# Optimization experiments

Measured on AMD Instinct MI355X. Metric: run time of the kernel, lower is better.

The kernel has to match this reference:

```python
import jax, jax.numpy as jnp
import numpy as np

N = 32768   # total nodes
E = 524288  # directed edges
F = 128     # input features
H = 128     # hidden width
G = 64      # graphs in batch (N//G = 512 nodes each)


def _lin(key, fan_in, fan_out):
    return jax.random.normal(key, (fan_in, fan_out), jnp.float32) / np.sqrt(fan_in)


def setup_inputs() -> dict:
    key = jax.random.key(0)
    ks = jax.random.split(key, 16)
    d = {}
    d["x"] = jax.random.normal(ks[0], (N, F), jnp.float32)
    d["edge_index"] = jax.random.randint(ks[1], (2, E), 0, N, dtype=jnp.int64)
    d["batch"] = (jnp.arange(N, dtype=jnp.int64) // (N // G))  # sorted, equal-size graphs
    # GCNConv 1 / 2
    d["W1"] = _lin(ks[2], F, H); d["b1"] = jnp.zeros((H,), jnp.float32)
    d["W2"] = _lin(ks[3], H, H); d["b2"] = jnp.zeros((H,), jnp.float32)
    # GraphSelfAttention (per-graph Q/K/V self-attention)
    d["Wq"] = _lin(ks[4], H, H); d["bq"] = jnp.zeros((H,), jnp.float32)
    d["Wk"] = _lin(ks[5], H, H); d["bk"] = jnp.zeros((H,), jnp.float32)
    d["Wv"] = _lin(ks[6], H, H); d["bv"] = jnp.zeros((H,), jnp.float32)
    # MLP head
    d["Wh1"] = _lin(ks[7], H, 64); d["bh1"] = jnp.zeros((64,), jnp.float32)
    d["Wh2"] = _lin(ks[8], 64, 1); d["bh2"] = jnp.zeros((1,), jnp.float32)
    return d


def gcn_conv(x, src, dst, W, b, num_nodes):
    """PyG-style GCNConv: D^{-1/2}(A+I)D^{-1/2} x W + b (self-loops already in src/dst)."""
    h = x @ W                                                    # [N, out]
    deg = jax.ops.segment_sum(jnp.ones_like(dst, dtype=h.dtype), dst,
                              num_segments=num_nodes)            # [N]
    dinv = jax.lax.rsqrt(jnp.maximum(deg, 1.0))
    norm = dinv[src] * dinv[dst]                                 # [E+N]
    msg = h[src] * norm[:, None]                                 # gather
    return jax.ops.segment_sum(msg, dst, num_segments=num_nodes) + b  # scatter-add


def reference(x, edge_index, batch, W1, b1, W2, b2, Wq, bq, Wk, bk, Wv, bv,
              Wh1, bh1, Wh2, bh2):
    num_nodes = x.shape[0]
    loop = jnp.arange(num_nodes, dtype=edge_index.dtype)
    src = jnp.concatenate([edge_index[0], loop])
    dst = jnp.concatenate([edge_index[1], loop])

    x = x.astype(jnp.float32)
    h = jax.nn.relu(gcn_conv(x, src, dst, W1, b1, num_nodes))    # dropout: eval mode (identity)
    h = jax.nn.relu(gcn_conv(h, src, dst, W2, b2, num_nodes))

    # batch = arange // n (equal-size sorted segments) -> dense reshape is exact
    n = num_nodes // G
    hg = h.reshape(G, n, H)                                      # [G, n, H]
    q = hg @ Wq + bq
    k = hg @ Wk + bk
    v = hg @ Wv + bv
    scores = jnp.einsum("gnd,gmd->gnm", q, k) / np.sqrt(H)       # [G, n, n]
    attn = jax.nn.softmax(scores, axis=-1)
    pooled = jnp.einsum("gnm,gmd->gnd", attn, v).mean(axis=1)    # [G, H]

    out = jax.nn.relu(pooled @ Wh1 + bh1) @ Wh2 + bh2            # [G, 1]
    return out
```

## Files before the change

kernel.cpp:

```cpp
#include <hip/hip_runtime.h>
#include <hip/hip_fp16.h>
#include <hip/hip_bf16.h>

#define NN 32768
#define GG 64
#define NPG 512
#define HD 128
#define MAXD 64
#define RSQRT_H 0.08838834764831845f

typedef _Float16 f16;
typedef __attribute__((ext_vector_type(8))) _Float16 f16x8;
typedef __attribute__((ext_vector_type(4))) float f32x4;

__global__ void k_fill(const int* __restrict__ src, const int* __restrict__ dst,
                       int* __restrict__ cursor, int* __restrict__ ell, int E) {
    int e = blockIdx.x * 256 + threadIdx.x;
    if (e < E) {
        int d = dst[e];
        int slot = atomicAdd(&cursor[d], 1);
        if (slot < MAXD) ell[d * MAXD + slot] = src[e];
    }
}

#define FMA_ROW(r, av, wv) \
    acc[r][0] += (av)*(wv).x; acc[r][1] += (av)*(wv).y; \
    acc[r][2] += (av)*(wv).z; acc[r][3] += (av)*(wv).w;

__global__ __launch_bounds__(256) void k_gemm_h(
    const float* __restrict__ A, const float* __restrict__ W,
    __half* __restrict__ out, int M)
{
    __shared__ float Al[64][132];
    __shared__ float Wt[128][68];
    int t = threadIdx.x;
    int row0 = blockIdx.x * 64;
    int col0 = blockIdx.y * 64;

    const float4* A4 = (const float4*)(A + (size_t)row0 * HD);
#pragma unroll
    for (int i = 0; i < 8; ++i) {
        int idx = t + 256 * i;
        *(float4*)&Al[idx >> 5][(idx & 31) * 4] = A4[idx];
    }
    const float4* W4 = (const float4*)W;
#pragma unroll
    for (int i = 0; i < 8; ++i) {
        int idx = t + 256 * i;
        int k = idx >> 4, cq = idx & 15;
        *(float4*)&Wt[k][cq * 4] = W4[k * 32 + (col0 >> 2) + cq];
    }
    __syncthreads();

    int cg = t & 15, rg = t >> 4;
    float acc[4][4] = {{0.f}};
#pragma unroll 2
    for (int kk = 0; kk < 128; kk += 4) {
        float4 a0 = *(const float4*)&Al[rg * 4 + 0][kk];
        float4 a1 = *(const float4*)&Al[rg * 4 + 1][kk];
        float4 a2 = *(const float4*)&Al[rg * 4 + 2][kk];
        float4 a3 = *(const float4*)&Al[rg * 4 + 3][kk];
        float4 w0 = *(const float4*)&Wt[kk + 0][cg * 4];
        float4 w1 = *(const float4*)&Wt[kk + 1][cg * 4];
        float4 w2 = *(const float4*)&Wt[kk + 2][cg * 4];
        float4 w3 = *(const float4*)&Wt[kk + 3][cg * 4];
        FMA_ROW(0, a0.x, w0) FMA_ROW(0, a0.y, w1) FMA_ROW(0, a0.z, w2) FMA_ROW(0, a0.w, w3)
        FMA_ROW(1, a1.x, w0) FMA_ROW(1, a1.y, w1) FMA_ROW(1, a1.z, w2) FMA_ROW(1, a1.w, w3)
        FMA_ROW(2, a2.x, w0) FMA_ROW(2, a2.y, w1) FMA_ROW(2, a2.z, w2) FMA_ROW(2, a2.w, w3)
        FMA_ROW(3, a3.x, w0) FMA_ROW(3, a3.y, w1) FMA_ROW(3, a3.z, w2) FMA_ROW(3, a3.w, w3)
    }
#pragma unroll
    for (int r = 0; r < 4; ++r) {
        int row = row0 + rg * 4 + r;
        __half2 p01, p23;
        p01.x = __float2half(acc[r][0]); p01.y = __float2half(acc[r][1]);
        p23.x = __float2half(acc[r][2]); p23.y = __float2half(acc[r][3]);
        __half2* o = (__half2*)&out[(size_t)row * HD + col0 + cg * 4];
        o[0] = p01; o[1] = p23;
    }
}

__global__ __launch_bounds__(256) void k_gemm_qk(
    const float* __restrict__ A,
    const float* __restrict__ Wq, const float* __restrict__ bq,
    const float* __restrict__ Wk, const float* __restrict__ bk,
    __half* __restrict__ qout, __half* __restrict__ kout)
{
    __shared__ float Al[64][132];
    __shared__ float Wt[128][68];
    int t = threadIdx.x;
    int row0 = blockIdx.x * 64;
    int col0 = blockIdx.y * 64;
    int cg = t & 15, rg = t >> 4;

    const float4* A4 = (const float4*)(A + (size_t)row0 * HD);
#pragma unroll
    for (int i = 0; i < 8; ++i) {
        int idx = t + 256 * i;
        *(float4*)&Al[idx >> 5][(idx & 31) * 4] = A4[idx];
    }
    const float4* Wq4 = (const float4*)Wq;
#pragma unroll
    for (int i = 0; i < 8; ++i) {
        int idx = t + 256 * i;
        int k = idx >> 4, cq = idx & 15;
        *(float4*)&Wt[k][cq * 4] = Wq4[k * 32 + (col0 >> 2) + cq];
    }
    __syncthreads();

    {
        float acc[4][4] = {{0.f}};
#pragma unroll 2
        for (int kk = 0; kk < 128; kk += 4) {
            float4 a0 = *(const float4*)&Al[rg * 4 + 0][kk];
            float4 a1 = *(const float4*)&Al[rg * 4 + 1][kk];
            float4 a2 = *(const float4*)&Al[rg * 4 + 2][kk];
            float4 a3 = *(const float4*)&Al[rg * 4 + 3][kk];
            float4 w0 = *(const float4*)&Wt[kk + 0][cg * 4];
            float4 w1 = *(const float4*)&Wt[kk + 1][cg * 4];
            float4 w2 = *(const float4*)&Wt[kk + 2][cg * 4];
            float4 w3 = *(const float4*)&Wt[kk + 3][cg * 4];
            FMA_ROW(0, a0.x, w0) FMA_ROW(0, a0.y, w1) FMA_ROW(0, a0.z, w2) FMA_ROW(0, a0.w, w3)
            FMA_ROW(1, a1.x, w0) FMA_ROW(1, a1.y, w1) FMA_ROW(1, a1.z, w2) FMA_ROW(1, a1.w, w3)
            FMA_ROW(2, a2.x, w0) FMA_ROW(2, a2.y, w1) FMA_ROW(2, a2.z, w2) FMA_ROW(2, a2.w, w3)
            FMA_ROW(3, a3.x, w0) FMA_ROW(3, a3.y, w1) FMA_ROW(3, a3.z, w2) FMA_ROW(3, a3.w, w3)
        }
        int c = col0 + cg * 4;
        float b0 = bq[c], b1 = bq[c+1], b2 = bq[c+2], b3 = bq[c+3];
#pragma unroll
        for (int r = 0; r < 4; ++r) {
            int row = row0 + rg * 4 + r;
            __half2 p01, p23;
            p01.x = __float2half(acc[r][0] + b0); p01.y = __float2half(acc[r][1] + b1);
            p23.x = __float2half(acc[r][2] + b2); p23.y = __float2half(acc[r][3] + b3);
            __half2* o = (__half2*)&qout[(size_t)row * HD + c];
            o[0] = p01; o[1] = p23;
        }
    }
    __syncthreads();
    const float4* Wk4 = (const float4*)Wk;
#pragma unroll
    for (int i = 0; i < 8; ++i) {
        int idx = t + 256 * i;
        int k = idx >> 4, cq = idx & 15;
        *(float4*)&Wt[k][cq * 4] = Wk4[k * 32 + (col0 >> 2) + cq];
    }
    __syncthreads();

    float acc[4][4] = {{0.f}};
#pragma unroll 2
    for (int kk = 0; kk < 128; kk += 4) {
        float4 a0 = *(const float4*)&Al[rg * 4 + 0][kk];
        float4 a1 = *(const float4*)&Al[rg * 4 + 1][kk];
        float4 a2 = *(const float4*)&Al[rg * 4 + 2][kk];
        float4 a3 = *(const float4*)&Al[rg * 4 + 3][kk];
        float4 w0 = *(const float4*)&Wt[kk + 0][cg * 4];
        float4 w1 = *(const float4*)&Wt[kk + 1][cg * 4];
        float4 w2 = *(const float4*)&Wt[kk + 2][cg * 4];
        float4 w3 = *(const float4*)&Wt[kk + 3][cg * 4];
        FMA_ROW(0, a0.x, w0) FMA_ROW(0, a0.y, w1) FMA_ROW(0, a0.z, w2) FMA_ROW(0, a0.w, w3)
        FMA_ROW(1, a1.x, w0) FMA_ROW(1, a1.y, w1) FMA_ROW(1, a1.z, w2) FMA_ROW(1, a1.w, w3)
        FMA_ROW(2, a2.x, w0) FMA_ROW(2, a2.y, w1) FMA_ROW(2, a2.z, w2) FMA_ROW(2, a2.w, w3)
        FMA_ROW(3, a3.x, w0) FMA_ROW(3, a3.y, w1) FMA_ROW(3, a3.z, w2) FMA_ROW(3, a3.w, w3)
    }
    {
        int c = col0 + cg * 4;
        float b0 = bk[c], b1 = bk[c+1], b2 = bk[c+2], b3 = bk[c+3];
#pragma unroll
        for (int r = 0; r < 4; ++r) {
            int row = row0 + rg * 4 + r;
            __half2 p01, p23;
            p01.x = __float2half(acc[r][0] + b0); p01.y = __float2half(acc[r][1] + b1);
            p23.x = __float2half(acc[r][2] + b2); p23.y = __float2half(acc[r][3] + b3);
            __half2* o = (__half2*)&kout[(size_t)row * HD + c];
            o[0] = p01; o[1] = p23;
        }
    }
}

__global__ __launch_bounds__(256) void k_agg(
    const __half* __restrict__ tmat, const int* __restrict__ cursor,
    const int* __restrict__ ell, const float* __restrict__ bias,
    float* __restrict__ hout)
{
    int t = threadIdx.x;
    int i = blockIdx.x * 4 + (t >> 6);
    int lane = t & 63;
    int cnt = min(cursor[i], MAXD);
    float di = rsqrtf((float)(cnt + 1));
    float2 sv = __half22float2(((const __half2*)(tmat + (size_t)i * HD))[lane]);
    float acc0 = sv.x * (di * di);
    float acc1 = sv.y * (di * di);
    const int* row = ell + (size_t)i * MAXD;
    int e = 0;
    for (; e + 2 <= cnt; e += 2) {
        int s0 = row[e], s1 = row[e + 1];
        float w0 = rsqrtf((float)(min(cursor[s0], MAXD) + 1)) * di;
        float w1 = rsqrtf((float)(min(cursor[s1], MAXD) + 1)) * di;
        float2 v0 = __half22float2(((const __half2*)(tmat + (size_t)s0 * HD))[lane]);
        float2 v1 = __half22float2(((const __half2*)(tmat + (size_t)s1 * HD))[lane]);
        acc0 += v0.x * w0 + v1.x * w1;
        acc1 += v0.y * w0 + v1.y * w1;
    }
    if (e < cnt) {
        int s0 = row[e];
        float w0 = rsqrtf((float)(min(cursor[s0], MAXD) + 1)) * di;
        float2 v0 = __half22float2(((const __half2*)(tmat + (size_t)s0 * HD))[lane]);
        acc0 += v0.x * w0;
        acc1 += v0.y * w0;
    }
    int f = lane * 2;
    *(float2*)&hout[(size_t)i * HD + f] =
        make_float2(fmaxf(acc0 + bias[f], 0.f), fmaxf(acc1 + bias[f + 1], 0.f));
}

__global__ __launch_bounds__(256, 2) void k_attn(
    const __half* __restrict__ qh,
    const __half* __restrict__ kh,
    float* __restrict__ wpart)
{
    __shared__ f16 Kl[64][136];
    __shared__ float wlp[4][512];
    int t = threadIdx.x;
    int g = blockIdx.x >> 3;
    int qt = blockIdx.x & 7;
    int w = t >> 6, lane = t & 63;
    int lr = lane & 15, lu = lane >> 4;
    int qrow0 = g * NPG + qt * 64;

    f16x8 aq[4];
    {
        const f16* qp = (const f16*)qh + (size_t)(qrow0 + w * 16 + lr) * HD + lu * 8;
#pragma unroll
        for (int ks = 0; ks < 4; ++ks)
            aq[ks] = *(const f16x8*)(qp + ks * 32);
    }

    f32x4 p[8][4];
#pragma unroll
    for (int mt = 0; mt < 8; ++mt) {
        __syncthreads();
        {
            const float4* ks4 = (const float4*)(kh + (size_t)(g * NPG + mt * 64) * HD);
#pragma unroll
            for (int i = 0; i < 4; ++i) {
                int idx = t + 256 * i;
                int row = idx >> 4, cq = idx & 15;
                *(float4*)&Kl[row][cq * 8] = ks4[row * 16 + cq];
            }
        }
        __syncthreads();
#pragma unroll
        for (int ni = 0; ni < 4; ++ni) {
            f32x4 acc = {0.f, 0.f, 0.f, 0.f};
#pragma unroll
            for (int ks = 0; ks < 4; ++ks) {
                f16x8 b = *(const f16x8*)&Kl[ni * 16 + lr][ks * 32 + lu * 8];
                acc = __builtin_amdgcn_mfma_f32_16x16x32_f16(aq[ks], b, acc, 0, 0, 0);
            }
            p[mt][ni] = acc;
        }
    }

    float mrow[4], linv[4];
#pragma unroll
    for (int j = 0; j < 4; ++j) {
        float m = p[0][0][j];
#pragma unroll
        for (int mt = 0; mt < 8; ++mt)
#pragma unroll
            for (int ni = 0; ni < 4; ++ni) m = fmaxf(m, p[mt][ni][j]);
        m = fmaxf(m, __shfl_xor(m, 1));
        m = fmaxf(m, __shfl_xor(m, 2));
        m = fmaxf(m, __shfl_xor(m, 4));
        m = fmaxf(m, __shfl_xor(m, 8));
        mrow[j] = m;
    }
#pragma unroll
    for (int mt = 0; mt < 8; ++mt)
#pragma unroll
        for (int ni = 0; ni < 4; ++ni)
#pragma unroll
            for (int j = 0; j < 4; ++j)
                p[mt][ni][j] = __expf((p[mt][ni][j] - mrow[j]) * RSQRT_H);
#pragma unroll
    for (int j = 0; j < 4; ++j) {
        float l = 0.f;
#pragma unroll
        for (int mt = 0; mt < 8; ++mt)
#pragma unroll
            for (int ni = 0; ni < 4; ++ni) l += p[mt][ni][j];
        l += __shfl_xor(l, 1);
        l += __shfl_xor(l, 2);
        l += __shfl_xor(l, 4);
        l += __shfl_xor(l, 8);
        linv[j] = 1.f / l;
    }
#pragma unroll
    for (int mt = 0; mt < 8; ++mt)
#pragma unroll
        for (int ni = 0; ni < 4; ++ni) {
            float pc = p[mt][ni][0] * linv[0] + p[mt][ni][1] * linv[1]
                     + p[mt][ni][2] * linv[2] + p[mt][ni][3] * linv[3];
            pc += __shfl_xor(pc, 16);
            pc += __shfl_xor(pc, 32);
            if (lu == 0) wlp[w][mt * 64 + ni * 16 + lr] = pc;
        }
    __syncthreads();
    float* wp = wpart + ((size_t)(g * 8 + qt)) * NPG;
    wp[t] = (wlp[0][t] + wlp[1][t] + wlp[2][t] + wlp[3][t]) * (1.f / NPG);
    wp[t + 256] = (wlp[0][t + 256] + wlp[1][t + 256] + wlp[2][t + 256]
                 + wlp[3][t + 256]) * (1.f / NPG);
}

__global__ __launch_bounds__(128) void k_pool(
    const float* __restrict__ wpart, const float* __restrict__ h,
    float* __restrict__ upart)
{
    __shared__ float wloc[64];
    int b = blockIdx.x;
    int g = b >> 3, ch = b & 7;
    int t = threadIdx.x;
    if (t < 64) {
        float w = 0.f;
#pragma unroll
        for (int qt = 0; qt < 8; ++qt)
            w += wpart[((size_t)(g * 8 + qt)) * NPG + ch * 64 + t];
        wloc[t] = w;
    }
    __syncthreads();
    const float* hg = h + ((size_t)g * NPG + ch * 64) * HD;
    float u = 0.f;
#pragma unroll 4
    for (int m = 0; m < 64; ++m) u += wloc[m] * hg[m * HD + t];
    upart[(size_t)(ch * GG + g) * HD + t] = u;
}

__global__ __launch_bounds__(128) void k_head2(
    const float* __restrict__ upart,
    const float* __restrict__ Wv, const float* __restrict__ bv,
    const float* __restrict__ Wh1, const float* __restrict__ bh1,
    const float* __restrict__ Wh2, const float* __restrict__ bh2,
    float* __restrict__ out)
{
    __shared__ float ul[128];
    __shared__ float pl[128];
    __shared__ float r1l[64];
    int g = blockIdx.x, t = threadIdx.x;
    float ud = 0.f;
#pragma unroll
    for (int ch = 0; ch < 8; ++ch) ud += upart[(size_t)(ch * GG + g) * HD + t];
    ul[t] = ud;
    __syncthreads();
    float pv = bv[t];
    for (int d = 0; d < HD; ++d) pv += ul[d] * Wv[d * HD + t];
    pl[t] = pv;
    __syncthreads();
    if (t < 64) {
        float r1 = bh1[t];
        for (int d = 0; d < HD; ++d) r1 += pl[d] * Wh1[d * 64 + t];
        r1l[t] = fmaxf(r1, 0.f);
    }
    __syncthreads();
    if (t == 0) {
        float o = bh2[0];
        for (int j = 0; j < 64; ++j) o += r1l[j] * Wh2[j];
        out[g] = o;
    }
}

extern "C" void kernel_launch(void* const* d_in, const int* in_sizes, int n_in,
                              void* d_out, int out_size, void* d_ws, size_t ws_size,
                              hipStream_t stream) {
    const float* x   = (const float*)d_in[0];
    const int* edge  = (const int*)d_in[1];
    const float* W1  = (const float*)d_in[3];
    const float* b1  = (const float*)d_in[4];
    const float* W2  = (const float*)d_in[5];
    const float* b2  = (const float*)d_in[6];
    const float* Wq  = (const float*)d_in[7];
    const float* bq  = (const float*)d_in[8];
    const float* Wk  = (const float*)d_in[9];
    const float* bk  = (const float*)d_in[10];
    const float* Wv  = (const float*)d_in[11];
    const float* bv  = (const float*)d_in[12];
    const float* Wh1 = (const float*)d_in[13];
    const float* bh1 = (const float*)d_in[14];
    const float* Wh2 = (const float*)d_in[15];
    const float* bh2 = (const float*)d_in[16];
    float* out = (float*)d_out;

    int E = in_sizes[1] / 2;
    const int* src = edge;
    const int* dst = edge + E;

    float* tbuf = (float*)d_ws;
    float* hbuf = tbuf + (size_t)NN * HD;
    float* r3   = hbuf + (size_t)NN * HD;
    float* wpart = r3 + (size_t)NN * HD;
    int* cursor = (int*)(wpart + GG * 8 * NPG);
    __half* tmat = (__half*)tbuf;
    __half* qh   = (__half*)tbuf;
    __half* kh   = qh + (size_t)NN * HD;
    int* ell    = (int*)r3;
    float* upart = r3;

    int eb = (E + 255) / 256;
    dim3 ggrid(NN / 64, 2);

    hipMemsetAsync(cursor, 0, NN * sizeof(int), stream);
    k_fill<<<eb, 256, 0, stream>>>(src, dst, cursor, ell, E);

    k_gemm_h<<<ggrid, 256, 0, stream>>>(x, W1, tmat, NN);
    k_agg<<<NN / 4, 256, 0, stream>>>(tmat, cursor, ell, b1, hbuf);
    k_gemm_h<<<ggrid, 256, 0, stream>>>(hbuf, W2, tmat, NN);
    k_agg<<<NN / 4, 256, 0, stream>>>(tmat, cursor, ell, b2, hbuf);
    k_gemm_qk<<<ggrid, 256, 0, stream>>>(hbuf, Wq, bq, Wk, bk, qh, kh);
    k_attn<<<GG * 8, 256, 0, stream>>>(qh, kh, wpart);
    k_pool<<<GG * 8, 128, 0, stream>>>(wpart, hbuf, upart);
    k_head2<<<GG, 128, 0, stream>>>(upart, Wv, bv, Wh1, bh1, Wh2, bh2, out);
}
```

Measured before the change: 297.3 us.

## Replace FP32 SIMT GEMMs with MFMA f16 GEMMs and store hidden state in half

Replaces the scalar FP32 FMA GEMM kernels with a templated MFMA 16x16x32 f16 kernel. Each block now computes a full 64x128 output tile, using weights pre-transposed to f16 by a new prep kernel. The aggregation output and pooling input change from float to half, which halves that buffer's traffic. The cost is f16 rounding of the hidden activations, one extra small kernel launch, and Q and K now being computed in two separate launches.

After: 262.1 us. -11.9%, faster.

```diff
diff --git a/kernel.cpp b/kernel.cpp
--- a/kernel.cpp
+++ b/kernel.cpp
@@ -10,6 +10,7 @@
 #define RSQRT_H 0.08838834764831845f
 
 typedef _Float16 f16;
+typedef __attribute__((ext_vector_type(4))) _Float16 f16x4;
 typedef __attribute__((ext_vector_type(8))) _Float16 f16x8;
 typedef __attribute__((ext_vector_type(4))) float f32x4;
 
@@ -23,165 +24,94 @@
     }
 }
 
-#define FMA_ROW(r, av, wv) \
-    acc[r][0] += (av)*(wv).x; acc[r][1] += (av)*(wv).y; \
-    acc[r][2] += (av)*(wv).z; acc[r][3] += (av)*(wv).w;
-
-__global__ __launch_bounds__(256) void k_gemm_h(
-    const float* __restrict__ A, const float* __restrict__ W,
-    __half* __restrict__ out, int M)
-{
-    __shared__ float Al[64][132];
-    __shared__ float Wt[128][68];
+__global__ void k_wprep(const float* __restrict__ W1, const float* __restrict__ W2,
+                        const float* __restrict__ Wq, const float* __restrict__ Wk,
+                        f16* __restrict__ wt) {
+    const float* Ws[4] = {W1, W2, Wq, Wk};
+    int k = blockIdx.x, wsel = blockIdx.y, n = threadIdx.x;
+    float v = Ws[wsel][k * HD + n];
+    wt[(size_t)wsel * HD * HD + n * HD + k] = (f16)v;
+}
+
+template<int AF32, int BIAS>
+__global__ __launch_bounds__(256) void k_mgemm(
+    const void* __restrict__ Ain, const f16* __restrict__ WT,
+    const float* __restrict__ bias, f16* __restrict__ out)
+{
+    __shared__ f16 Al[64][136];
+    __shared__ f16 Wl[128][136];
     int t = threadIdx.x;
     int row0 = blockIdx.x * 64;
-    int col0 = blockIdx.y * 64;
-
-    const float4* A4 = (const float4*)(A + (size_t)row0 * HD);
+    int w = t >> 6, lane = t & 63, lr = lane & 15, lu = lane >> 4;
+
+    if (AF32) {
+        const float4* A32 = (const float4*)((const float*)Ain + (size_t)row0 * HD);
+#pragma unroll
+        for (int i = 0; i < 8; ++i) {
+            int idx = t + 256 * i;
+            int r = idx >> 5, c4 = idx & 31;
+            float4 v = A32[idx];
+            f16x4 h = {(f16)v.x, (f16)v.y, (f16)v.z, (f16)v.w};
+            *(f16x4*)&Al[r][c4 * 4] = h;
+        }
+    } else {
+        const float4* A16 = (const float4*)((const f16*)Ain + (size_t)row0 * HD);
+#pragma unroll
+        for (int i = 0; i < 4; ++i) {
+            int idx = t + 256 * i;
+            int r = idx >> 4, cq = idx & 15;
+            *(float4*)&Al[r][cq * 8] = A16[idx];
+        }
+    }
+    const float4* W4 = (const float4*)WT;
 #pragma unroll
     for (int i = 0; i < 8; ++i) {
         int idx = t + 256 * i;
-        *(float4*)&Al[idx >> 5][(idx & 31) * 4] = A4[idx];
-    }
-    const float4* W4 = (const float4*)W;
-#pragma unroll
-    for (int i = 0; i < 8; ++i) {
+        int n = idx >> 4, cq = idx & 15;
+        *(float4*)&Wl[n][cq * 8] = W4[idx];
+    }
+    __syncthreads();
+
+    f16x8 aq[4];
+#pragma unroll
+    for (int ks = 0; ks < 4; ++ks)
+        aq[ks] = *(const f16x8*)&Al[w * 16 + lr][ks * 32 + lu * 8];
+
+    f32x4 acc[8];
+#pragma unroll
+    for (int ni = 0; ni < 8; ++ni) {
+        f32x4 c = {0.f, 0.f, 0.f, 0.f};
+#pragma unroll
+        for (int ks = 0; ks < 4; ++ks) {
+            f16x8 b = *(const f16x8*)&Wl[ni * 16 + lr][ks * 32 + lu * 8];
+            c = __builtin_amdgcn_mfma_f32_16x16x32_f16(aq[ks], b, c, 0, 0, 0);
+        }
+        acc[ni] = c;
+    }
+
+    __syncthreads();
+#pragma unroll
+    for (int ni = 0; ni < 8; ++ni)
+#pragma unroll
+        for (int j = 0; j < 4; ++j) {
+            float v = acc[ni][j];
+            if (BIAS) v += bias[ni * 16 + lr];
+            Al[w * 16 + lu * 4 + j][ni * 16 + lr] = (f16)v;
+        }
+    __syncthreads();
+    float4* O4 = (float4*)(out + (size_t)row0 * HD);
+#pragma unroll
+    for (int i = 0; i < 4; ++i) {
         int idx = t + 256 * i;
-        int k = idx >> 4, cq = idx & 15;
-        *(float4*)&Wt[k][cq * 4] = W4[k * 32 + (col0 >> 2) + cq];
-    }
-    __syncthreads();
-
-    int cg = t & 15, rg = t >> 4;
-    float acc[4][4] = {{0.f}};
-#pragma unroll 2
-    for (int kk = 0; kk < 128; kk += 4) {
-        float4 a0 = *(const float4*)&Al[rg * 4 + 0][kk];
-        float4 a1 = *(const float4*)&Al[rg * 4 + 1][kk];
-        float4 a2 = *(const float4*)&Al[rg * 4 + 2][kk];
-        float4 a3 = *(const float4*)&Al[rg * 4 + 3][kk];
-        float4 w0 = *(const float4*)&Wt[kk + 0][cg * 4];
-        float4 w1 = *(const float4*)&Wt[kk + 1][cg * 4];
-        float4 w2 = *(const float4*)&Wt[kk + 2][cg * 4];
-        float4 w3 = *(const float4*)&Wt[kk + 3][cg * 4];
-        FMA_ROW(0, a0.x, w0) FMA_ROW(0, a0.y, w1) FMA_ROW(0, a0.z, w2) FMA_ROW(0, a0.w, w3)
-        FMA_ROW(1, a1.x, w0) FMA_ROW(1, a1.y, w1) FMA_ROW(1, a1.z, w2) FMA_ROW(1, a1.w, w3)
-        FMA_ROW(2, a2.x, w0) FMA_ROW(2, a2.y, w1) FMA_ROW(2, a2.z, w2) FMA_ROW(2, a2.w, w3)
-        FMA_ROW(3, a3.x, w0) FMA_ROW(3, a3.y, w1) FMA_ROW(3, a3.z, w2) FMA_ROW(3, a3.w, w3)
-    }
-#pragma unroll
-    for (int r = 0; r < 4; ++r) {
-        int row = row0 + rg * 4 + r;
-        __half2 p01, p23;
-        p01.x = __float2half(acc[r][0]); p01.y = __float2half(acc[r][1]);
-        p23.x = __float2half(acc[r][2]); p23.y = __float2half(acc[r][3]);
-        __half2* o = (__half2*)&out[(size_t)row * HD + col0 + cg * 4];
-        o[0] = p01; o[1] = p23;
-    }
-}
-
-__global__ __launch_bounds__(256) void k_gemm_qk(
-    const float* __restrict__ A,
-    const float* __restrict__ Wq, const float* __restrict__ bq,
-    const float* __restrict__ Wk, const float* __restrict__ bk,
-    __half* __restrict__ qout, __half* __restrict__ kout)
-{
-    __shared__ float Al[64][132];
-    __shared__ float Wt[128][68];
-    int t = threadIdx.x;
-    int row0 = blockIdx.x * 64;
-    int col0 = blockIdx.y * 64;
-    int cg = t & 15, rg = t >> 4;
-
-    const float4* A4 = (const float4*)(A + (size_t)row0 * HD);
-#pragma unroll
-    for (int i = 0; i < 8; ++i) {
-        int idx = t + 256 * i;
-        *(float4*)&Al[idx >> 5][(idx & 31) * 4] = A4[idx];
-    }
-    const float4* Wq4 = (const float4*)Wq;
-#pragma unroll
-    for (int i = 0; i < 8; ++i) {
-        int idx = t + 256 * i;
-        int k = idx >> 4, cq = idx & 15;
-        *(float4*)&Wt[k][cq * 4] = Wq4[k * 32 + (col0 >> 2) + cq];
-    }
-    __syncthreads();
-
-    {
-        float acc[4][4] = {{0.f}};
-#pragma unroll 2
-        for (int kk = 0; kk < 128; kk += 4) {
-            float4 a0 = *(const float4*)&Al[rg * 4 + 0][kk];
-            float4 a1 = *(const float4*)&Al[rg * 4 + 1][kk];
-            float4 a2 = *(const float4*)&Al[rg * 4 + 2][kk];
-            float4 a3 = *(const float4*)&Al[rg * 4 + 3][kk];
-            float4 w0 = *(const float4*)&Wt[kk + 0][cg * 4];
-            float4 w1 = *(const float4*)&Wt[kk + 1][cg * 4];
-            float4 w2 = *(const float4*)&Wt[kk + 2][cg * 4];
-            float4 w3 = *(const float4*)&Wt[kk + 3][cg * 4];
-            FMA_ROW(0, a0.x, w0) FMA_ROW(0, a0.y, w1) FMA_ROW(0, a0.z, w2) FMA_ROW(0, a0.w, w3)
-            FMA_ROW(1, a1.x, w0) FMA_ROW(1, a1.y, w1) FMA_ROW(1, a1.z, w2) FMA_ROW(1, a1.w, w3)
-            FMA_ROW(2, a2.x, w0) FMA_ROW(2, a2.y, w1) FMA_ROW(2, a2.z, w2) FMA_ROW(2, a2.w, w3)
-            FMA_ROW(3, a3.x, w0) FMA_ROW(3, a3.y, w1) FMA_ROW(3, a3.z, w2) FMA_ROW(3, a3.w, w3)
-        }
-        int c = col0 + cg * 4;
-        float b0 = bq[c], b1 = bq[c+1], b2 = bq[c+2], b3 = bq[c+3];
-#pragma unroll
-        for (int r = 0; r < 4; ++r) {
-            int row = row0 + rg * 4 + r;
-            __half2 p01, p23;
-            p01.x = __float2half(acc[r][0] + b0); p01.y = __float2half(acc[r][1] + b1);
-            p23.x = __float2half(acc[r][2] + b2); p23.y = __float2half(acc[r][3] + b3);
-            __half2* o = (__half2*)&qout[(size_t)row * HD + c];
-            o[0] = p01; o[1] = p23;
-        }
-    }
-    __syncthreads();
-    const float4* Wk4 = (const float4*)Wk;
-#pragma unroll
-    for (int i = 0; i < 8; ++i) {
-        int idx = t + 256 * i;
-        int k = idx >> 4, cq = idx & 15;
-        *(float4*)&Wt[k][cq * 4] = Wk4[k * 32 + (col0 >> 2) + cq];
-    }
-    __syncthreads();
-
-    float acc[4][4] = {{0.f}};
-#pragma unroll 2
-    for (int kk = 0; kk < 128; kk += 4) {
-        float4 a0 = *(const float4*)&Al[rg * 4 + 0][kk];
-        float4 a1 = *(const float4*)&Al[rg * 4 + 1][kk];
-        float4 a2 = *(const float4*)&Al[rg * 4 + 2][kk];
-        float4 a3 = *(const float4*)&Al[rg * 4 + 3][kk];
-        float4 w0 = *(const float4*)&Wt[kk + 0][cg * 4];
-        float4 w1 = *(const float4*)&Wt[kk + 1][cg * 4];
-        float4 w2 = *(const float4*)&Wt[kk + 2][cg * 4];
-        float4 w3 = *(const float4*)&Wt[kk + 3][cg * 4];
-        FMA_ROW(0, a0.x, w0) FMA_ROW(0, a0.y, w1) FMA_ROW(0, a0.z, w2) FMA_ROW(0, a0.w, w3)
-        FMA_ROW(1, a1.x, w0) FMA_ROW(1, a1.y, w1) FMA_ROW(1, a1.z, w2) FMA_ROW(1, a1.w, w3)
-        FMA_ROW(2, a2.x, w0) FMA_ROW(2, a2.y, w1) FMA_ROW(2, a2.z, w2) FMA_ROW(2, a2.w, w3)
-        FMA_ROW(3, a3.x, w0) FMA_ROW(3, a3.y, w1) FMA_ROW(3, a3.z, w2) FMA_ROW(3, a3.w, w3)
-    }
-    {
-        int c = col0 + cg * 4;
-        float b0 = bk[c], b1 = bk[c+1], b2 = bk[c+2], b3 = bk[c+3];
-#pragma unroll
-        for (int r = 0; r < 4; ++r) {
-            int row = row0 + rg * 4 + r;
-            __half2 p01, p23;
-            p01.x = __float2half(acc[r][0] + b0); p01.y = __float2half(acc[r][1] + b1);
-            p23.x = __float2half(acc[r][2] + b2); p23.y = __float2half(acc[r][3] + b3);
-            __half2* o = (__half2*)&kout[(size_t)row * HD + c];
-            o[0] = p01; o[1] = p23;
-        }
+        int r = idx >> 4, cq = idx & 15;
+        O4[idx] = *(float4*)&Al[r][cq * 8];
     }
 }
 
 __global__ __launch_bounds__(256) void k_agg(
     const __half* __restrict__ tmat, const int* __restrict__ cursor,
     const int* __restrict__ ell, const float* __restrict__ bias,
-    float* __restrict__ hout)
+    __half* __restrict__ hout)
 {
     int t = threadIdx.x;
     int i = blockIdx.x * 4 + (t >> 6);
@@ -210,8 +140,10 @@
         acc1 += v0.y * w0;
     }
     int f = lane * 2;
-    *(float2*)&hout[(size_t)i * HD + f] =
-        make_float2(fmaxf(acc0 + bias[f], 0.f), fmaxf(acc1 + bias[f + 1], 0.f));
+    __half2 o;
+    o.x = __float2half(fmaxf(acc0 + bias[f], 0.f));
+    o.y = __float2half(fmaxf(acc1 + bias[f + 1], 0.f));
+    ((__half2*)(hout + (size_t)i * HD))[lane] = o;
 }
 
 __global__ __launch_bounds__(256, 2) void k_attn(
@@ -314,7 +246,7 @@
 }
 
 __global__ __launch_bounds__(128) void k_pool(
-    const float* __restrict__ wpart, const float* __restrict__ h,
+    const float* __restrict__ wpart, const __half* __restrict__ h,
     float* __restrict__ upart)
 {
     __shared__ float wloc[64];
@@ -329,10 +261,10 @@
         wloc[t] = w;
     }
     __syncthreads();
-    const float* hg = h + ((size_t)g * NPG + ch * 64) * HD;
+    const __half* hg = h + ((size_t)g * NPG + ch * 64) * HD;
     float u = 0.f;
 #pragma unroll 4
-    for (int m = 0; m < 64; ++m) u += wloc[m] * hg[m * HD + t];
+    for (int m = 0; m < 64; ++m) u += wloc[m] * __half2float(hg[m * HD + t]);
     upart[(size_t)(ch * GG + g) * HD + t] = u;
 }
 
@@ -395,27 +327,32 @@
     const int* dst = edge + E;
 
     float* tbuf = (float*)d_ws;
-    float* hbuf = tbuf + (size_t)NN * HD;
-    float* r3   = hbuf + (size_t)NN * HD;
+    float* hbr  = tbuf + (size_t)NN * HD;
+    float* r3   = hbr + (size_t)NN * HD;
     float* wpart = r3 + (size_t)NN * HD;
     int* cursor = (int*)(wpart + GG * 8 * NPG);
+    f16* wtb    = (f16*)(cursor + NN);
     __half* tmat = (__half*)tbuf;
     __half* qh   = (__half*)tbuf;
     __half* kh   = qh + (size_t)NN * HD;
+    __half* hbuf = (__half*)hbr;
     int* ell    = (int*)r3;
     float* upart = r3;
+    f16* W1T = wtb, *W2T = wtb + HD * HD, *WqT = wtb + 2 * HD * HD,
+       * WkT = wtb + 3 * HD * HD;
 
     int eb = (E + 255) / 256;
-    dim3 ggrid(NN / 64, 2);
 
     hipMemsetAsync(cursor, 0, NN * sizeof(int), stream);
     k_fill<<<eb, 256, 0, stream>>>(src, dst, cursor, ell, E);
-
-    k_gemm_h<<<ggrid, 256, 0, stream>>>(x, W1, tmat, NN);
+    k_wprep<<<dim3(HD, 4), HD, 0, stream>>>(W1, W2, Wq, Wk, wtb);
+
+    k_mgemm<1, 0><<<NN / 64, 256, 0, stream>>>(x, W1T, nullptr, (f16*)tmat);
     k_agg<<<NN / 4, 256, 0, stream>>>(tmat, cursor, ell, b1, hbuf);
-    k_gemm_h<<<ggrid, 256, 0, stream>>>(hbuf, W2, tmat, NN);
+    k_mgemm<0, 0><<<NN / 64, 256, 0, stream>>>(hbuf, W2T, nullptr, (f16*)tmat);
     k_agg<<<NN / 4, 256, 0, stream>>>(tmat, cursor, ell, b2, hbuf);
-    k_gemm_qk<<<ggrid, 256, 0, stream>>>(hbuf, Wq, bq, Wk, bk, qh, kh);
+    k_mgemm<0, 1><<<NN / 64, 256, 0, stream>>>(hbuf, WqT, bq, (f16*)qh);
+    k_mgemm<0, 1><<<NN / 64, 256, 0, stream>>>(hbuf, WkT, bk, (f16*)kh);
     k_attn<<<GG * 8, 256, 0, stream>>>(qh, kh, wpart);
     k_pool<<<GG * 8, 128, 0, stream>>>(wpart, hbuf, upart);
     k_head2<<<GG, 128, 0, stream>>>(upart, Wv, bv, Wh1, bh1, Wh2, bh2, out);
```
